# Optimization experiments

Hardware: AMD Instinct MI355X
Metric: run time of the kernel (lower is better)

## Reference

```python
import jax, jax.numpy as jnp
import numpy as np

KERNEL = 3  # kernel_size from init_kwargs


def _unfold(x, k):
    """torch.nn.functional.unfold with padding=k//2, stride=1.
    Returns [b, c*k*k, h*w] with torch's ordering: index = c*(k*k) + kh*k + kw.
    """
    b, c, h, w = x.shape
    p = k // 2
    xp = jnp.pad(x, ((0, 0), (0, 0), (p, p), (p, p)))
    # fixed k*k = 9 slices (small static loop, not a data-dim loop)
    cols = jnp.stack(
        [xp[:, :, i:i + h, j:j + w] for i in range(k) for j in range(k)],
        axis=2,
    )  # [b, c, k*k, h, w]
    return cols.reshape(b, c * k * k, h * w)


def setup_inputs() -> dict:
    key = jax.random.key(0)
    k1, k2 = jax.random.split(key)
    x = jax.random.normal(k1, (8, 64, 128, 128), dtype=jnp.float32)
    # memory parameter: torch.rand -> uniform [0, 1), shape [c*k*k, out_channels]
    memory = jax.random.uniform(k2, (64 * KERNEL * KERNEL, 128), dtype=jnp.float32)
    return {"x": x, "memory": memory}


def reference(x, memory):
    b, c, h, w = x.shape
    cols = _unfold(x, KERNEL)                 # [b, c*k*k, h*w]
    cols = jax.nn.softmax(cols, axis=1)       # softmax over unfolded patch dim
    out = jnp.einsum('ki,bkl->bil', memory, cols)  # [b, out_ch, h*w]
    return out.reshape(b, memory.shape[1], h, w)
```

## Files before the change

### kernel.cpp

```cpp
#include <hip/hip_runtime.h>
#include <stdint.h>


#define Cn 64
#define Hn 128
#define Wn 128
#define OC 128
#define HW (Hn * Wn)

typedef __attribute__((ext_vector_type(8))) short bf16x8_t;
typedef __attribute__((ext_vector_type(16))) float f32x16_t;

__device__ inline unsigned short f2bf(float f) {
    union { float f; uint32_t u; } v; v.f = f;
    uint32_t u = v.u;
    u += 0x7fffu + ((u >> 16) & 1u);
    return (unsigned short)(u >> 16);
}
__device__ inline float bf_lo(uint32_t u) {
    union { uint32_t u; float f; } v; v.u = u << 16;
    return v.f;
}
__device__ inline float bf_hi(uint32_t u) {
    union { uint32_t u; float f; } v; v.u = u & 0xffff0000u;
    return v.f;
}

__global__ void prep_b2(const float* __restrict__ mem, uint4* __restrict__ Bt2) {
    int u = blockIdx.x * 256 + threadIdx.x;
    int n = u & 127;
    int cid = u >> 7;
    int hi = cid & 1;
    int kc = cid >> 1;
    int q = kc >> 2, cblk = kc & 3;
    unsigned short h8[8];
#pragma unroll
    for (int j = 0; j < 8; j++) {
        int c = cblk * 16 + hi * 8 + j;
        h8[j] = f2bf(mem[(c * 9 + q) * OC + n]);
    }
    Bt2[cid * 128 + n] = *(const uint4*)h8;
}

__global__ __launch_bounds__(256, 2) void convf(const float* __restrict__ x,
                                                const uint4* __restrict__ Bt2,
                                                float* __restrict__ out) {
    __shared__ __align__(16) uint4 EtL[324 * 8];
    __shared__ float Sh[324];
    __shared__ float Zt[256];

    int bid = blockIdx.x;
    int b = bid >> 6;
    int ty = (bid >> 3) & 7, tx = bid & 7;
    int h0 = ty * 16, w0 = tx * 16;
    int t = threadIdx.x;
    uint32_t* Lu = (uint32_t*)EtL;

    const float* xb = x + (size_t)b * Cn * HW;

#pragma unroll
    for (int i = 0; i < 9; i++) {
        int u = i * 256 + t;
        int qx = u & 3;
        int w2 = u >> 2;
        int py = w2 % 18;
        int cp = w2 / 18;
        int gy = h0 - 1 + py;
        int g = cp >> 2, jj = cp & 3;
        int pb = py * 18 + 1 + qx * 4;
        uint32_t pk0, pk1, pk2, pk3;
        if (gy >= 0 && gy < Hn) {
            const float* r0 = xb + (size_t)(2 * cp) * HW + gy * Wn + w0 + qx * 4;
            float4 v0 = *(const float4*)r0;
            float4 v1 = *(const float4*)(r0 + HW);
            pk0 = (uint32_t)f2bf(__expf(v0.x)) | ((uint32_t)f2bf(__expf(v1.x)) << 16);
            pk1 = (uint32_t)f2bf(__expf(v0.y)) | ((uint32_t)f2bf(__expf(v1.y)) << 16);
            pk2 = (uint32_t)f2bf(__expf(v0.z)) | ((uint32_t)f2bf(__expf(v1.z)) << 16);
            pk3 = (uint32_t)f2bf(__expf(v0.w)) | ((uint32_t)f2bf(__expf(v1.w)) << 16);
        } else {
            pk0 = pk1 = pk2 = pk3 = 0x3F803F80u;
        }
        Lu[(pb + 0) * 32 + (((g ^ ((pb + 0) & 7)) << 2) | jj)] = pk0;
        Lu[(pb + 1) * 32 + (((g ^ ((pb + 1) & 7)) << 2) | jj)] = pk1;
        Lu[(pb + 2) * 32 + (((g ^ ((pb + 2) & 7)) << 2) | jj)] = pk2;
        Lu[(pb + 3) * 32 + (((g ^ ((pb + 3) & 7)) << 2) | jj)] = pk3;
    }

#pragma unroll
    for (int i = 0; i < 5; i++) {
        int u = i * 256 + t;
        if (u < 1152) {
            int side = u & 1;
            int v = u >> 1;
            int py = v % 18;
            int cp = v / 18;
            int gy = h0 - 1 + py;
            int gx = side ? (w0 + 16) : (w0 - 1);
            int p = py * 18 + side * 17;
            int g = cp >> 2, jj = cp & 3;
            uint32_t pk;
            if (gy >= 0 && gy < Hn && gx >= 0 && gx < Wn) {
                const float* r0 = xb + (size_t)(2 * cp) * HW + gy * Wn + gx;
                pk = (uint32_t)f2bf(__expf(r0[0])) | ((uint32_t)f2bf(__expf(r0[HW])) << 16);
            } else {
                pk = 0x3F803F80u;
            }
            Lu[p * 32 + (((g ^ (p & 7)) << 2) | jj)] = pk;
        }
    }
    __syncthreads();

#pragma unroll
    for (int pi = 0; pi < 2; pi++) {
        int p = pi * 256 + t;
        if (p < 324) {
            float s = 0.f;
#pragma unroll
            for (int k = 0; k < 8; k++) {
                uint4 q = EtL[p * 8 + ((k + t) & 7)];
                s += bf_lo(q.x) + bf_hi(q.x) + bf_lo(q.y) + bf_hi(q.y)
                   + bf_lo(q.z) + bf_hi(q.z) + bf_lo(q.w) + bf_hi(q.w);
            }
            Sh[p] = s;
        }
    }
    __syncthreads();

    {
        int zy = t >> 4, zx = t & 15;
        float z = 0.f;
#pragma unroll
        for (int dy = 0; dy < 3; dy++)
#pragma unroll
            for (int dx = 0; dx < 3; dx++)
                z += Sh[(zy + dy) * 18 + (zx + dx)];
        Zt[t] = 1.0f / z;
    }
    __syncthreads();

    int lane = t & 63, wv = t >> 6;
    int l31 = lane & 31, hi = lane >> 5;
    int x0v = l31 & 15;
    int y0[2];
    y0[0] = (wv * 2 + 0) * 2 + (l31 >> 4);
    y0[1] = (wv * 2 + 1) * 2 + (l31 >> 4);

    f32x16_t acc[2][4];
#pragma unroll
    for (int j = 0; j < 2; j++)
#pragma unroll
        for (int g = 0; g < 4; g++)
#pragma unroll
            for (int r = 0; r < 16; r++) acc[j][g][r] = 0.f;

    bf16x8_t Wf[3][4], Ef[3][2];

    auto loadW = [&](int kc, int s) {
        const uint4* bp = Bt2 + (size_t)((kc * 2 + hi) * 128 + l31);
#pragma unroll
        for (int g = 0; g < 4; g++)
            Wf[s][g] = *(const bf16x8_t*)(bp + g * 32);
    };
    auto loadE = [&](int kc, int s) {
        int q = kc >> 2, cblk = kc & 3;
        int kh = q / 3, kw = q - kh * 3;
        int g = cblk * 2 + hi;
#pragma unroll
        for (int j = 0; j < 2; j++) {
            int pix = (y0[j] + kh) * 18 + (x0v + kw);
            Ef[s][j] = *(const bf16x8_t*)&EtL[pix * 8 + (g ^ (pix & 7))];
        }
    };

    loadW(0, 0); loadE(0, 0);
    loadW(1, 1); loadE(1, 1);
    loadW(2, 2); loadE(2, 2);
#pragma unroll
    for (int kc = 0; kc < 36; kc++) {
        int s = kc % 3;
#pragma unroll
        for (int g = 0; g < 4; g++)
#pragma unroll
            for (int j = 0; j < 2; j++)
                acc[j][g] = __builtin_amdgcn_mfma_f32_32x32x16_bf16(
                    Wf[s][g], Ef[s][j], acc[j][g], 0, 0, 0);
        if (kc + 3 < 36) { loadW(kc + 3, s); loadE(kc + 3, s); }
    }

#pragma unroll
    for (int j = 0; j < 2; j++) {
        float zi = Zt[(wv * 2 + j) * 32 + l31];
        float* ob = out + (size_t)b * OC * HW + (h0 + y0[j]) * Wn + (w0 + x0v)
                  + (size_t)(4 * hi) * HW;
#pragma unroll
        for (int g = 0; g < 4; g++) {
#pragma unroll
            for (int r = 0; r < 16; r++) {
                int nrel = g * 32 + (r & 3) + 8 * (r >> 2);
                ob[(size_t)nrel * HW] = acc[j][g][r] * zi;
            }
        }
    }
}

extern "C" void kernel_launch(void* const* d_in, const int* in_sizes, int n_in,
                              void* d_out, int out_size, void* d_ws, size_t ws_size,
                              hipStream_t stream) {
    const float* x = (const float*)d_in[0];
    const float* mem = (const float*)d_in[1];
    float* out = (float*)d_out;

    uint4* Bt2 = (uint4*)d_ws;

    prep_b2<<<36, 256, 0, stream>>>(mem, Bt2);
    convf<<<512, 256, 0, stream>>>(x, Bt2, out);
}
```

Measured before the change: 121.9 us.

## Shrink tiles to 8x16, split output channels across waves, rework halo load

Each block now covers an 8x16 pixel tile with 512 threads. The 8 waves split the 128 output channels into four 32-wide groups and the tile rows into two pairs, so each wave holds only 2 accumulators instead of 8. The halo load is rewritten so each thread reads 8 channels as float4s and writes full 16-byte LDS granules. The swizzle changes to use pix>>1, and block indices are remapped to interleave batches. The aim is to cut register pressure, raise occupancy and use wider LDS stores, at the cost of more halo overhead per tile (10x18 vs 18x18 for half the pixels) and reloading the exp'd input across waves.

```diff
diff --git a/kernel.cpp b/kernel.cpp
--- a/kernel.cpp
+++ b/kernel.cpp
@@ -42,91 +42,95 @@
     Bt2[cid * 128 + n] = *(const uint4*)h8;
 }
 
-__global__ __launch_bounds__(256, 2) void convf(const float* __restrict__ x,
+__global__ __launch_bounds__(512, 4) void convf(const float* __restrict__ x,
                                                 const uint4* __restrict__ Bt2,
                                                 float* __restrict__ out) {
-    __shared__ __align__(16) uint4 EtL[324 * 8];
-    __shared__ float Sh[324];
-    __shared__ float Zt[256];
-
-    int bid = blockIdx.x;
-    int b = bid >> 6;
-    int ty = (bid >> 3) & 7, tx = bid & 7;
-    int h0 = ty * 16, w0 = tx * 16;
+    __shared__ __align__(16) uint4 EtL[180 * 8];
+    __shared__ float Sh[180];
+    __shared__ float Zt[128];
+
+    int bid0 = blockIdx.x;
+    int bid = ((bid0 & 7) << 7) | (bid0 >> 3);
+    int b = bid >> 7;
+    int ty = (bid >> 3) & 15, tx = bid & 7;
+    int h0 = ty * 8, w0 = tx * 16;
     int t = threadIdx.x;
-    uint32_t* Lu = (uint32_t*)EtL;
 
     const float* xb = x + (size_t)b * Cn * HW;
-
-#pragma unroll
-    for (int i = 0; i < 9; i++) {
-        int u = i * 256 + t;
-        int qx = u & 3;
-        int w2 = u >> 2;
-        int py = w2 % 18;
-        int cp = w2 / 18;
+    const uint4 PAD = make_uint4(0x3F803F80u, 0x3F803F80u, 0x3F803F80u, 0x3F803F80u);
+
+    if (t < 480) {
+        int qs = t % 6;
+        int v6 = t / 6;
+        int py = v6 % 10;
+        int g  = v6 / 10;
         int gy = h0 - 1 + py;
-        int g = cp >> 2, jj = cp & 3;
-        int pb = py * 18 + 1 + qx * 4;
-        uint32_t pk0, pk1, pk2, pk3;
-        if (gy >= 0 && gy < Hn) {
-            const float* r0 = xb + (size_t)(2 * cp) * HW + gy * Wn + w0 + qx * 4;
-            float4 v0 = *(const float4*)r0;
-            float4 v1 = *(const float4*)(r0 + HW);
-            pk0 = (uint32_t)f2bf(__expf(v0.x)) | ((uint32_t)f2bf(__expf(v1.x)) << 16);
-            pk1 = (uint32_t)f2bf(__expf(v0.y)) | ((uint32_t)f2bf(__expf(v1.y)) << 16);
-            pk2 = (uint32_t)f2bf(__expf(v0.z)) | ((uint32_t)f2bf(__expf(v1.z)) << 16);
-            pk3 = (uint32_t)f2bf(__expf(v0.w)) | ((uint32_t)f2bf(__expf(v1.w)) << 16);
+        bool inrow = (gy >= 0) & (gy < Hn);
+        int xg = w0 - 4 + qs * 4;
+        const float* base = xb + (size_t)(8 * g) * HW + (size_t)gy * Wn + xg;
+
+        if (qs >= 1 && qs <= 4) {
+            if (inrow) {
+                float4 v[8];
+#pragma unroll
+                for (int k = 0; k < 8; k++)
+                    v[k] = *(const float4*)(base + (size_t)k * HW);
+#pragma unroll
+                for (int i = 0; i < 4; i++) {
+                    uint32_t wd[4];
+#pragma unroll
+                    for (int j = 0; j < 4; j++) {
+                        float a = ((const float*)&v[2 * j])[i];
+                        float c = ((const float*)&v[2 * j + 1])[i];
+                        wd[j] = (uint32_t)f2bf(__expf(a)) | ((uint32_t)f2bf(__expf(c)) << 16);
+                    }
+                    int p = py * 18 + (qs - 1) * 4 + 1 + i;
+                    EtL[p * 8 + (g ^ ((p >> 1) & 7))] = *(const uint4*)wd;
+                }
+            } else {
+#pragma unroll
+                for (int i = 0; i < 4; i++) {
+                    int p = py * 18 + (qs - 1) * 4 + 1 + i;
+                    EtL[p * 8 + (g ^ ((p >> 1) & 7))] = PAD;
+                }
+            }
         } else {
-            pk0 = pk1 = pk2 = pk3 = 0x3F803F80u;
-        }
-        Lu[(pb + 0) * 32 + (((g ^ ((pb + 0) & 7)) << 2) | jj)] = pk0;
-        Lu[(pb + 1) * 32 + (((g ^ ((pb + 1) & 7)) << 2) | jj)] = pk1;
-        Lu[(pb + 2) * 32 + (((g ^ ((pb + 2) & 7)) << 2) | jj)] = pk2;
-        Lu[(pb + 3) * 32 + (((g ^ ((pb + 3) & 7)) << 2) | jj)] = pk3;
-    }
-
-#pragma unroll
-    for (int i = 0; i < 5; i++) {
-        int u = i * 256 + t;
-        if (u < 1152) {
-            int side = u & 1;
-            int v = u >> 1;
-            int py = v % 18;
-            int cp = v / 18;
-            int gy = h0 - 1 + py;
-            int gx = side ? (w0 + 16) : (w0 - 1);
-            int p = py * 18 + side * 17;
-            int g = cp >> 2, jj = cp & 3;
-            uint32_t pk;
-            if (gy >= 0 && gy < Hn && gx >= 0 && gx < Wn) {
-                const float* r0 = xb + (size_t)(2 * cp) * HW + gy * Wn + gx;
-                pk = (uint32_t)f2bf(__expf(r0[0])) | ((uint32_t)f2bf(__expf(r0[HW])) << 16);
-            } else {
-                pk = 0x3F803F80u;
+            int side = (qs == 5);
+            int p = py * 18 + (side ? 17 : 0);
+            bool real = inrow && (side ? (tx < 7) : (tx > 0));
+            uint4 gran = PAD;
+            if (real) {
+                float4 v[8];
+#pragma unroll
+                for (int k = 0; k < 8; k++)
+                    v[k] = *(const float4*)(base + (size_t)k * HW);
+                uint32_t wd[4];
+#pragma unroll
+                for (int j = 0; j < 4; j++) {
+                    float a = side ? ((const float*)&v[2 * j])[0]     : ((const float*)&v[2 * j])[3];
+                    float c = side ? ((const float*)&v[2 * j + 1])[0] : ((const float*)&v[2 * j + 1])[3];
+                    wd[j] = (uint32_t)f2bf(__expf(a)) | ((uint32_t)f2bf(__expf(c)) << 16);
+                }
+                gran = *(const uint4*)wd;
             }
-            Lu[p * 32 + (((g ^ (p & 7)) << 2) | jj)] = pk;
+            EtL[p * 8 + (g ^ ((p >> 1) & 7))] = gran;
         }
     }
     __syncthreads();
 
-#pragma unroll
-    for (int pi = 0; pi < 2; pi++) {
-        int p = pi * 256 + t;
-        if (p < 324) {
-            float s = 0.f;
-#pragma unroll
-            for (int k = 0; k < 8; k++) {
-                uint4 q = EtL[p * 8 + ((k + t) & 7)];
-                s += bf_lo(q.x) + bf_hi(q.x) + bf_lo(q.y) + bf_hi(q.y)
-                   + bf_lo(q.z) + bf_hi(q.z) + bf_lo(q.w) + bf_hi(q.w);
-            }
-            Sh[p] = s;
-        }
+    if (t < 180) {
+        float s = 0.f;
+#pragma unroll
+        for (int k = 0; k < 8; k++) {
+            uint4 q = EtL[t * 8 + ((k + t) & 7)];
+            s += bf_lo(q.x) + bf_hi(q.x) + bf_lo(q.y) + bf_hi(q.y)
+               + bf_lo(q.z) + bf_hi(q.z) + bf_lo(q.w) + bf_hi(q.w);
+        }
+        Sh[t] = s;
     }
     __syncthreads();
 
-    {
+    if (t < 128) {
         int zy = t >> 4, zx = t & 15;
         float z = 0.f;
 #pragma unroll
@@ -138,37 +142,35 @@
     }
     __syncthreads();
 
-    int lane = t & 63, wv = t >> 6;
+    int lane = t & 63;
+    int wid = t >> 6;
+    int wo = wid & 3;
+    int wp = wid >> 2;
     int l31 = lane & 31, hi = lane >> 5;
     int x0v = l31 & 15;
     int y0[2];
-    y0[0] = (wv * 2 + 0) * 2 + (l31 >> 4);
-    y0[1] = (wv * 2 + 1) * 2 + (l31 >> 4);
-
-    f32x16_t acc[2][4];
+    y0[0] = (wp * 2 + 0) * 2 + (l31 >> 4);
+    y0[1] = (wp * 2 + 1) * 2 + (l31 >> 4);
+
+    f32x16_t acc[2];
 #pragma unroll
     for (int j = 0; j < 2; j++)
 #pragma unroll
-        for (int g = 0; g < 4; g++)
-#pragma unroll
-            for (int r = 0; r < 16; r++) acc[j][g][r] = 0.f;
-
-    bf16x8_t Wf[3][4], Ef[3][2];
+        for (int r = 0; r < 16; r++) acc[j][r] = 0.f;
+
+    bf16x8_t Wf[3], Ef[3][2];
 
     auto loadW = [&](int kc, int s) {
-        const uint4* bp = Bt2 + (size_t)((kc * 2 + hi) * 128 + l31);
-#pragma unroll
-        for (int g = 0; g < 4; g++)
-            Wf[s][g] = *(const bf16x8_t*)(bp + g * 32);
+        Wf[s] = *(const bf16x8_t*)(Bt2 + (size_t)((kc * 2 + hi) * 128 + wo * 32 + l31));
     };
     auto loadE = [&](int kc, int s) {
         int q = kc >> 2, cblk = kc & 3;
         int kh = q / 3, kw = q - kh * 3;
-        int g = cblk * 2 + hi;
+        int ge = cblk * 2 + hi;
 #pragma unroll
         for (int j = 0; j < 2; j++) {
             int pix = (y0[j] + kh) * 18 + (x0v + kw);
-            Ef[s][j] = *(const bf16x8_t*)&EtL[pix * 8 + (g ^ (pix & 7))];
+            Ef[s][j] = *(const bf16x8_t*)&EtL[pix * 8 + (ge ^ ((pix >> 1) & 7))];
         }
     };
 
@@ -179,26 +181,21 @@
     for (int kc = 0; kc < 36; kc++) {
         int s = kc % 3;
 #pragma unroll
-        for (int g = 0; g < 4; g++)
-#pragma unroll
-            for (int j = 0; j < 2; j++)
-                acc[j][g] = __builtin_amdgcn_mfma_f32_32x32x16_bf16(
-                    Wf[s][g], Ef[s][j], acc[j][g], 0, 0, 0);
+        for (int j = 0; j < 2; j++)
+            acc[j] = __builtin_amdgcn_mfma_f32_32x32x16_bf16(
+                Wf[s], Ef[s][j], acc[j], 0, 0, 0);
         if (kc + 3 < 36) { loadW(kc + 3, s); loadE(kc + 3, s); }
     }
 
 #pragma unroll
     for (int j = 0; j < 2; j++) {
-        float zi = Zt[(wv * 2 + j) * 32 + l31];
-        float* ob = out + (size_t)b * OC * HW + (h0 + y0[j]) * Wn + (w0 + x0v)
-                  + (size_t)(4 * hi) * HW;
-#pragma unroll
-        for (int g = 0; g < 4; g++) {
-#pragma unroll
-            for (int r = 0; r < 16; r++) {
-                int nrel = g * 32 + (r & 3) + 8 * (r >> 2);
-                ob[(size_t)nrel * HW] = acc[j][g][r] * zi;
-            }
+        float zi = Zt[(y0[j] << 4) | x0v];
+        float* ob = out + (size_t)b * OC * HW + (size_t)(wo * 32 + 4 * hi) * HW
+                  + (h0 + y0[j]) * Wn + (w0 + x0v);
+#pragma unroll
+        for (int r = 0; r < 16; r++) {
+            int nrel = (r & 3) + 8 * (r >> 2);
+            ob[(size_t)nrel * HW] = acc[j][r] * zi;
         }
     }
 }
@@ -213,5 +210,5 @@
     uint4* Bt2 = (uint4*)d_ws;
 
     prep_b2<<<36, 256, 0, stream>>>(mem, Bt2);
-    convf<<<512, 256, 0, stream>>>(x, Bt2, out);
-}
+    convf<<<1024, 512, 0, stream>>>(x, Bt2, out);
+}
```

New measurement: 112.4 us. -7.8%, faster.
